# Performance work log

Measured on AMD Instinct MI355X. Metric: run time of the kernel, lower is better.

Reference implementation:

```python
import jax, jax.numpy as jnp
import numpy as np

MASS = 1.5
DT = 0.01      # physics.refresh_rate
EPS = 1e-6
B, STATE, ACT, T, H = 2048, 12, 4, 128, 512

_NORM = np.zeros(STATE, dtype=np.float32)
_NORM[0] = 4.0 / np.pi; _NORM[1] = 0.5; _NORM[2] = 4.0 / np.pi
_NORM[3] = 0.1; _NORM[4] = 1.0 / 60.0; _NORM[5] = 1.0 / 60.0
_NORM = jnp.asarray(_NORM)  # indices 6:12 stay zero (predict only normalizes 0:6)


def _leaky(x):
    return jnp.where(x >= 0, x, 0.01 * x)


def _mlp(x, W0, b0, W1, b1, W2, b2, W3, b3):
    # 3 hidden LeakyReLU layers + linear head (dropout is eval-mode identity)
    h = _leaky(x @ W0 + b0)
    h = _leaky(h @ W1 + b1)
    h = _leaky(h @ W2 + b2)
    return h @ W3 + b3


def _L_EB(phi, theta, psi):
    cph, sph = jnp.cos(phi), jnp.sin(phi)
    cth, sth = jnp.cos(theta), jnp.sin(theta)
    cps, sps = jnp.cos(psi), jnp.sin(psi)
    r1 = jnp.stack([cth * cps, sph * sth * cps - cph * sps, cph * sth * cps + sph * sps], -1)
    r2 = jnp.stack([cth * sps, sph * sth * sps + cph * cps, cph * sth * sps - sph * cps], -1)
    r3 = jnp.stack([-sth, sph * cth, cph * cth], -1)
    return jnp.stack([r1, r2, r3], -2)  # [B,3,3]


def _derivs(x, forces, I_mat, I_inv):
    V = x[:, 3:6]
    phi, theta = x[:, 6], x[:, 7]
    psi = x[:, 8]
    omega = x[:, 9:12]
    Fv, M = forces[:, 0:3], forces[:, 3:6]
    dpos = jnp.einsum('bij,bj->bi', _L_EB(phi, theta, psi), V)
    dvel = Fv / MASS - jnp.cross(omega, V)
    tth = jnp.tan(theta)
    cth = jnp.clip(jnp.cos(theta), EPS)
    sph, cph = jnp.sin(phi), jnp.cos(phi)
    one, zero = jnp.ones_like(phi), jnp.zeros_like(phi)
    J = jnp.stack([
        jnp.stack([one, sph * tth, cph * tth], -1),
        jnp.stack([zero, cph, -sph], -1),
        jnp.stack([zero, sph / cth, cph / cth], -1)], -2)  # [B,3,3]
    datt = jnp.einsum('bij,bj->bi', J, omega)
    Iw = omega @ I_mat.T                       # I @ omega
    coriolis = jnp.cross(omega, Iw)
    domega = (M - coriolis) @ I_inv.T
    return jnp.concatenate([dpos, dvel, datt, domega], axis=1)


def _rk4(x, forces, I_mat, I_inv):
    f = lambda s: _derivs(s, forces, I_mat, I_inv)
    k1 = f(x)
    k2 = f(x + 0.5 * DT * k1)
    k3 = f(x + 0.5 * DT * k2)
    k4 = f(x + DT * k3)
    return x + (DT / 6.0) * (k1 + 2 * k2 + 2 * k3 + k4)


def _predict(x, act, W, I_mat, I_inv):
    norm_x = x * _NORM
    norm_act = (act - 1500.0) / 500.0
    fn = _mlp(jnp.concatenate([norm_x, norm_act], axis=1), *W)
    zeros = jnp.zeros_like(fn[:, 0])
    forces = jnp.stack([fn[:, 0] - 0.5,
                        fn[:, 1] * -0.4 - 10.0,
                        fn[:, 2] * 0.2 - 0.1,
                        zeros, zeros, zeros], axis=1)
    return forces, _rk4(x, forces, I_mat, I_inv)


def setup_inputs() -> dict:
    key = jax.random.key(0)
    ks = jax.random.split(key, 12)
    x_t = jax.random.normal(ks[0], (B, STATE), dtype=jnp.float32) * 0.1
    act_inps = jax.random.uniform(ks[1], (B, ACT, T), dtype=jnp.float32,
                                  minval=1000.0, maxval=2000.0)
    I_mat = jnp.asarray([[0.02, 0.001, 0.002],
                         [0.001, 0.03, 0.001],
                         [0.002, 0.001, 0.04]], dtype=jnp.float32)
    def lin(k, fi, fo):
        s = np.sqrt(2.0 / (fi + fo)).astype(np.float32)
        return jax.random.normal(k, (fi, fo), dtype=jnp.float32) * s
    dims = [(STATE + ACT, H), (H, H), (H, H), (H, 6)]
    W = {}
    for i, (fi, fo) in enumerate(dims):
        W[f'W{i}'] = lin(ks[2 + i], fi, fo)
        W[f'b{i}'] = jnp.zeros((fo,), dtype=jnp.float32)
    return dict(x_t=x_t, act_inps=act_inps, I_mat=I_mat, seq_len=T, **W)


def reference(x_t, act_inps, I_mat, W0, b0, W1, b1, W2, b2, W3, b3, seq_len):
    I_inv = jnp.linalg.inv(I_mat)
    W = (W0, b0, W1, b1, W2, b2, W3, b3)
    acts = jnp.transpose(act_inps[:, :, 1:seq_len], (2, 0, 1))  # [T-1,B,ACT]

    def step(x, act):
        forces, nx = _predict(x, act, W, I_mat, I_inv)
        return nx, (forces, nx)

    _, (forces_seq, x_seq) = jax.lax.scan(step, x_t, acts)
    stacked = jnp.concatenate([x_t[:, :, None], jnp.transpose(x_seq, (1, 2, 0))], axis=2)  # [B,12,T]
    stackedForces = jnp.transpose(forces_seq, (1, 2, 0))  # [B,6,T-1]
    return stackedForces, stacked
```

## Files before the change

### kernel.cpp

```cpp
#include <hip/hip_runtime.h>
#include <stdint.h>

typedef unsigned short u16;
typedef unsigned int   u32;
typedef __attribute__((ext_vector_type(8))) short short8;
typedef __attribute__((ext_vector_type(4))) float f32x4;

#define B_TOT   2048
#define HID     512
#define T_FULL  128
#define ROWS    32
#define NWG     (B_TOT / ROWS)
#define THREADS 512
#define NT      4

#define W0F_SZ  16384
#define W1F_SZ  262144
#define W3F_SZ  8192
#define WF_TOTAL (W0F_SZ + 2*W1F_SZ + W3F_SZ)

__device__ __forceinline__ u16 f2bf(float f){
  u32 u = __float_as_uint(f);
  u32 r = (u + 0x7FFFu + ((u >> 16) & 1u)) >> 16;
  return (u16)r;
}

__device__ __forceinline__ int lds_idx(int m, int k){
  int chunk = k >> 3;
  return m * 512 + ((chunk ^ (m & 7)) << 3) + (k & 7);
}

__global__ void wm_repack(const float* __restrict__ W0, const float* __restrict__ W1,
                          const float* __restrict__ W2, const float* __restrict__ W3,
                          u16* __restrict__ wf)
{
  int idx = blockIdx.x * blockDim.x + threadIdx.x;
  if (idx >= WF_TOTAL) return;
  int e = idx;
  if (e < W0F_SZ){
    int j = e & 7, l = (e >> 3) & 63, nt = e >> 9;
    int k = ((l >> 4) << 3) + j, n = (nt << 4) + (l & 15);
    wf[idx] = (k < 16) ? f2bf(W0[k * HID + n]) : (u16)0;
    return;
  }
  e -= W0F_SZ;
  if (e < W1F_SZ){
    int j = e & 7, l = (e >> 3) & 63, rest = e >> 9, kt = rest & 15, nt = rest >> 4;
    int k = (kt << 5) + ((l >> 4) << 3) + j, n = (nt << 4) + (l & 15);
    wf[idx] = f2bf(W1[k * HID + n]);
    return;
  }
  e -= W1F_SZ;
  if (e < W1F_SZ){
    int j = e & 7, l = (e >> 3) & 63, rest = e >> 9, kt = rest & 15, nt = rest >> 4;
    int k = (kt << 5) + ((l >> 4) << 3) + j, n = (nt << 4) + (l & 15);
    wf[idx] = f2bf(W2[k * HID + n]);
    return;
  }
  e -= W1F_SZ;
  {
    int j = e & 7, l = (e >> 3) & 63, kt = e >> 9;
    int k = (kt << 5) + ((l >> 4) << 3) + j, n = l & 15;
    wf[idx] = (n < 6) ? f2bf(W3[k * 6 + n]) : (u16)0;
  }
}

__device__ __forceinline__ void invert3(const float* a, float* inv){
  float d = a[0]*(a[4]*a[8]-a[5]*a[7]) - a[1]*(a[3]*a[8]-a[5]*a[6]) + a[2]*(a[3]*a[7]-a[4]*a[6]);
  float id = 1.0f / d;
  inv[0]=(a[4]*a[8]-a[5]*a[7])*id; inv[1]=(a[2]*a[7]-a[1]*a[8])*id; inv[2]=(a[1]*a[5]-a[2]*a[4])*id;
  inv[3]=(a[5]*a[6]-a[3]*a[8])*id; inv[4]=(a[0]*a[8]-a[2]*a[6])*id; inv[5]=(a[2]*a[3]-a[0]*a[5])*id;
  inv[6]=(a[3]*a[7]-a[4]*a[6])*id; inv[7]=(a[1]*a[6]-a[0]*a[7])*id; inv[8]=(a[0]*a[4]-a[1]*a[3])*id;
}

__device__ __forceinline__ void derivs(const float* x, const float* Fv,
                                       const float* I9, const float* Ii, float* dx)
{
  float V0=x[3], V1=x[4], V2=x[5];
  float phi=x[6], th=x[7], psi=x[8];
  float w0=x[9], w1=x[10], w2=x[11];
  float sph=__sinf(phi), cph=__cosf(phi);
  float sth=__sinf(th),  cth=__cosf(th);
  float sps=__sinf(psi), cps=__cosf(psi);
  float r00=cth*cps, r01=sph*sth*cps - cph*sps, r02=cph*sth*cps + sph*sps;
  float r10=cth*sps, r11=sph*sth*sps + cph*cps, r12=cph*sth*sps - sph*cps;
  float r20=-sth,    r21=sph*cth,               r22=cph*cth;
  dx[0]=r00*V0+r01*V1+r02*V2;
  dx[1]=r10*V0+r11*V1+r12*V2;
  dx[2]=r20*V0+r21*V1+r22*V2;
  const float invm = 1.0f/1.5f;
  dx[3]=Fv[0]*invm - (w1*V2 - w2*V1);
  dx[4]=Fv[1]*invm - (w2*V0 - w0*V2);
  dx[5]=Fv[2]*invm - (w0*V1 - w1*V0);
  float tth = sth / cth;
  float rc  = 1.0f / fmaxf(cth, 1e-6f);
  dx[6]= w0 + sph*tth*w1 + cph*tth*w2;
  dx[7]=      cph*w1     - sph*w2;
  dx[8]=      sph*rc*w1  + cph*rc*w2;
  float Iw0=I9[0]*w0+I9[1]*w1+I9[2]*w2;
  float Iw1=I9[3]*w0+I9[4]*w1+I9[5]*w2;
  float Iw2=I9[6]*w0+I9[7]*w1+I9[8]*w2;
  float c0=w1*Iw2-w2*Iw1, c1=w2*Iw0-w0*Iw2, c2=w0*Iw1-w1*Iw0;
  dx[9] = -(Ii[0]*c0+Ii[1]*c1+Ii[2]*c2);
  dx[10]= -(Ii[3]*c0+Ii[4]*c1+Ii[5]*c2);
  dx[11]= -(Ii[6]*c0+Ii[7]*c1+Ii[8]*c2);
}

__device__ __forceinline__ void rk4(float* X, const float* Fv, const float* I9, const float* Ii){
  float k1[12],k2[12],k3[12],k4[12],xt[12];
  derivs(X,Fv,I9,Ii,k1);
  #pragma unroll
  for (int c=0;c<12;++c) xt[c]=X[c]+0.005f*k1[c];
  derivs(xt,Fv,I9,Ii,k2);
  #pragma unroll
  for (int c=0;c<12;++c) xt[c]=X[c]+0.005f*k2[c];
  derivs(xt,Fv,I9,Ii,k3);
  #pragma unroll
  for (int c=0;c<12;++c) xt[c]=X[c]+0.01f*k3[c];
  derivs(xt,Fv,I9,Ii,k4);
  #pragma unroll
  for (int c=0;c<12;++c) X[c]+=(0.01f/6.0f)*(k1[c]+2.0f*k2[c]+2.0f*k3[c]+k4[c]);
}

__device__ __forceinline__ void build_input(u16* bufA, const float* X,
                                            const float* __restrict__ act,
                                            int b, int r, int t)
{
  float vin[16];
  vin[0]=X[0]*1.2732395447351628f;
  vin[1]=X[1]*0.5f;
  vin[2]=X[2]*1.2732395447351628f;
  vin[3]=X[3]*0.1f;
  vin[4]=X[4]*0.016666666666666666f;
  vin[5]=X[5]*0.016666666666666666f;
  #pragma unroll
  for (int c=6;c<12;++c) vin[c]=0.0f;
  #pragma unroll
  for (int a=0;a<4;++a)
    vin[12+a] = (act[(size_t)(b*4+a)*T_FULL + t] - 1500.0f) * 0.002f;
  #pragma unroll
  for (int p=0;p<16;++p){
    u32 pack = 0u;
    if (p < 8) pack = (u32)f2bf(vin[2*p]) | ((u32)f2bf(vin[2*p+1]) << 16);
    ((u32*)bufA)[lds_idx(r, 2*p) >> 1] = pack;
  }
}

template<int KT>
__device__ __forceinline__ void do_layer(const u16* __restrict__ bufIn,
                                         const u16* __restrict__ wfrag,
                                         const float* __restrict__ bias,
                                         u16* __restrict__ bufOut,
                                         int lane, int ntb)
{
  const int lm = lane & 15, half = lane >> 4;
  const int m0 = lm, m1 = 16 + lm;
  const int sw0 = m0 & 7, sw1 = m1 & 7;
  f32x4 acc0[NT], acc1[NT];
  #pragma unroll
  for (int i=0;i<NT;++i){ acc0[i]=(f32x4)0.0f; acc1[i]=(f32x4)0.0f; }

  const u16* wbase = wfrag + (((size_t)ntb*KT*64 + lane) << 3);

  if constexpr (KT == 1){
    short8 A0 = *(const short8*)(bufIn + m0*512 + ((half ^ sw0) << 3));
    short8 A1 = *(const short8*)(bufIn + m1*512 + ((half ^ sw1) << 3));
    short8 Bf[NT];
    #pragma unroll
    for (int i=0;i<NT;++i)
      Bf[i] = *(const short8*)(wbase + ((size_t)i << 9));
    #pragma unroll
    for (int i=0;i<NT;++i){
      acc0[i] = __builtin_amdgcn_mfma_f32_16x16x32_bf16(A0, Bf[i], acc0[i], 0, 0, 0);
      acc1[i] = __builtin_amdgcn_mfma_f32_16x16x32_bf16(A1, Bf[i], acc1[i], 0, 0, 0);
    }
  } else {
    static_assert(KT == 16, "KT must be 1 or 16");
    short8 Bf[2][4][NT];
    #pragma unroll
    for (int j=0;j<4;++j)
      #pragma unroll
      for (int i=0;i<NT;++i)
        Bf[0][j][i] = *(const short8*)(wbase + ((size_t)(i*KT + j) << 9));
    #pragma unroll
    for (int blk=0; blk<4; ++blk){
      const int cur = blk & 1, nxt = cur ^ 1;
      if (blk < 3){
        #pragma unroll
        for (int j=0;j<4;++j)
          #pragma unroll
          for (int i=0;i<NT;++i)
            Bf[nxt][j][i] = *(const short8*)(wbase + ((size_t)(i*KT + blk*4 + 4 + j) << 9));
      }
      short8 A0[4], A1[4];
      #pragma unroll
      for (int j=0;j<4;++j){
        const int cb = ((blk*4 + j) << 2) + half;
        A0[j] = *(const short8*)(bufIn + m0*512 + ((cb ^ sw0) << 3));
        A1[j] = *(const short8*)(bufIn + m1*512 + ((cb ^ sw1) << 3));
      }
      #pragma unroll
      for (int j=0;j<4;++j)
        #pragma unroll
        for (int i=0;i<NT;++i){
          acc0[i] = __builtin_amdgcn_mfma_f32_16x16x32_bf16(A0[j], Bf[cur][j][i], acc0[i], 0, 0, 0);
          acc1[i] = __builtin_amdgcn_mfma_f32_16x16x32_bf16(A1[j], Bf[cur][j][i], acc1[i], 0, 0, 0);
        }
    }
  }
  #pragma unroll
  for (int i=0;i<NT;++i){
    int n = ((ntb + i) << 4) + lm;
    float bv = bias[n];
    #pragma unroll
    for (int reg=0; reg<4; ++reg){
      int r0 = (half << 2) + reg, r1 = 16 + r0;
      float v0 = acc0[i][reg] + bv; v0 = (v0 >= 0.0f) ? v0 : 0.01f*v0;
      float v1 = acc1[i][reg] + bv; v1 = (v1 >= 0.0f) ? v1 : 0.01f*v1;
      bufOut[lds_idx(r0, n)] = f2bf(v0);
      bufOut[lds_idx(r1, n)] = f2bf(v1);
    }
  }
}

__global__ __launch_bounds__(THREADS, 2)
void wm_main(const float* __restrict__ x_t, const float* __restrict__ act,
             const float* __restrict__ Imat, const int* __restrict__ seqlen_p,
             const float* __restrict__ b0, const float* __restrict__ b1,
             const float* __restrict__ b2, const float* __restrict__ b3,
             const u16* __restrict__ wf, float* __restrict__ out)
{
  __shared__ u16 bufA[16384];
  __shared__ u16 bufB[16384];
  __shared__ float xstage[32*12*32];
  __shared__ float fstage[32*6*32];
  float* fscr = (float*)(bufA + 256);

  const int tid  = threadIdx.x;
  const int lane = tid & 63;
  const int wave = tid >> 6;
  const int ntb  = wave * NT;
  const int rowbase = blockIdx.x * ROWS;
  const int steps = seqlen_p[0] - 1;
  const int seqlen = steps + 1;

  const u16* w0f = wf;
  const u16* w1f = wf + W0F_SZ;
  const u16* w2f = w1f + W1F_SZ;
  const u16* w3f = w2f + W1F_SZ;

  float* outF = out;
  float* outX = out + (size_t)B_TOT * 6 * steps;

  float X[12];
  if (tid < ROWS){
    const int b = rowbase + tid;
    #pragma unroll
    for (int c=0;c<12;++c){
      float raw = x_t[b*12 + c];
      X[c] = raw;
      outX[(size_t)(b*12 + c)*seqlen] = raw;
    }
    build_input(bufA, X, act, b, tid, 1);
  }

  for (int s=0; s<steps; ++s){
    __syncthreads();
    do_layer<1 >(bufA, w0f, b0, bufB, lane, ntb);
    __syncthreads();
    do_layer<16>(bufB, w1f, b1, bufA, lane, ntb);
    __syncthreads();
    do_layer<16>(bufA, w2f, b2, bufB, lane, ntb);
    __syncthreads();
    const int slot = s & 31;
    if (wave == 0){
      const int lm = lane & 15, half = lane >> 4;
      const int m0 = lm, m1 = 16 + lm;
      const int sw0 = m0 & 7, sw1 = m1 & 7;
      short8 w3r[16];
      #pragma unroll
      for (int kt=0; kt<16; ++kt)
        w3r[kt] = *(const short8*)(w3f + (((size_t)kt*64 + lane) << 3));
      f32x4 a3_0 = (f32x4)0.0f, a3_1 = (f32x4)0.0f;
      #pragma unroll
      for (int kt=0; kt<16; ++kt){
        int cb = (kt << 2) + half;
        short8 x0 = *(const short8*)(bufB + m0*512 + ((cb ^ sw0) << 3));
        short8 x1 = *(const short8*)(bufB + m1*512 + ((cb ^ sw1) << 3));
        a3_0 = __builtin_amdgcn_mfma_f32_16x16x32_bf16(x0, w3r[kt], a3_0, 0, 0, 0);
        a3_1 = __builtin_amdgcn_mfma_f32_16x16x32_bf16(x1, w3r[kt], a3_1, 0, 0, 0);
      }
      const int c = lm;
      float bv = (c < 6) ? b3[c] : 0.0f;
      #pragma unroll
      for (int mt=0; mt<2; ++mt){
        #pragma unroll
        for (int reg=0; reg<4; ++reg){
          int rr = (mt << 4) + (half << 2) + reg;
          float fn = ((mt == 0) ? a3_0[reg] : a3_1[reg]) + bv;
          float f;
          if      (c == 0) f = fn - 0.5f;
          else if (c == 1) f = fn * -0.4f - 10.0f;
          else if (c == 2) f = fn * 0.2f - 0.1f;
          else             f = 0.0f;
          if (c < 6) fstage[(rr*6 + c)*32 + slot] = f;
          if (c < 3) fscr[rr*3 + c] = f;
        }
      }
      asm volatile("s_waitcnt lgkmcnt(0)" ::: "memory");
      if (tid < ROWS){
        const int b = rowbase + tid;
        float I9[9], Ii[9];
        #pragma unroll
        for (int i=0;i<9;++i) I9[i] = Imat[i];
        invert3(I9, Ii);
        float Fv[3] = { fscr[tid*3], fscr[tid*3+1], fscr[tid*3+2] };
        rk4(X, Fv, I9, Ii);
        #pragma unroll
        for (int cc=0;cc<12;++cc)
          xstage[(tid*12 + cc)*32 + slot] = X[cc];
        if (s + 1 < steps) build_input(bufA, X, act, b, tid, s + 2);
      }
    }
    if (slot == 31 || s == steps - 1){
      __syncthreads();
      const int cnt = slot + 1;
      const int sBase = s - slot;
      const int so = tid & 31;
      if (so < cnt){
        for (int i = tid; i < 384*32; i += THREADS){
          int pair = i >> 5;
          int row = pair / 12, c = pair - row*12;
          outX[(size_t)((rowbase + row)*12 + c)*seqlen + sBase + 1 + so]
              = xstage[pair*32 + so];
        }
        for (int i = tid; i < 192*32; i += THREADS){
          int pair = i >> 5;
          int row = pair / 6, c = pair - row*6;
          outF[(size_t)((rowbase + row)*6 + c)*steps + sBase + so]
              = fstage[pair*32 + so];
        }
      }
    }
  }
}

extern "C" void kernel_launch(void* const* d_in, const int* in_sizes, int n_in,
                              void* d_out, int out_size, void* d_ws, size_t ws_size,
                              hipStream_t stream)
{
  const float* x_t  = (const float*)d_in[0];
  const float* act  = (const float*)d_in[1];
  const float* Imat = (const float*)d_in[2];
  const int*   seqp = (const int*)d_in[3];
  const float* W0   = (const float*)d_in[4];
  const float* b0   = (const float*)d_in[5];
  const float* W1   = (const float*)d_in[6];
  const float* b1   = (const float*)d_in[7];
  const float* W2   = (const float*)d_in[8];
  const float* b2   = (const float*)d_in[9];
  const float* W3   = (const float*)d_in[10];
  const float* b3   = (const float*)d_in[11];
  u16* wfrag = (u16*)d_ws;

  hipLaunchKernelGGL(wm_repack, dim3((WF_TOTAL + 255)/256), dim3(256), 0, stream,
                     W0, W1, W2, W3, wfrag);
  hipLaunchKernelGGL(wm_main, dim3(NWG), dim3(THREADS), 0, stream,
                     x_t, act, Imat, seqp, b0, b1, b2, b3, wfrag, (float*)d_out);
}
```

Before: 5.351 ms.

## Double threads per block, halve per-wave N tiles, use 3-deep weight prefetch

Raises the workgroup from 512 to 1024 threads so each wave owns 2 instead of 4 output column tiles. The 4-block weight double buffer becomes a per-k-step triple-buffered prefetch of B fragments, which cuts register pressure. Launch bounds are raised so more waves can be resident to hide global weight load latency. The trade is shallower prefetch per wave and more waves contending for LDS. The rest of the kernel's thread-index mapping (ROWS=32 rows, staging loops) must stay valid for 16 waves, and that code is not visible.

```diff
diff --git a/kernel.cpp b/kernel.cpp
--- a/kernel.cpp
+++ b/kernel.cpp
@@ -11,8 +11,8 @@
 #define T_FULL  128
 #define ROWS    32
 #define NWG     (B_TOT / ROWS)
-#define THREADS 512
-#define NT      4
+#define THREADS 1024
+#define NT      2
 
 #define W0F_SZ  16384
 #define W1F_SZ  262144
@@ -176,36 +176,29 @@
     }
   } else {
     static_assert(KT == 16, "KT must be 1 or 16");
-    short8 Bf[2][4][NT];
-    #pragma unroll
-    for (int j=0;j<4;++j)
+    short8 Bf[3][NT];
+    #pragma unroll
+    for (int i=0;i<NT;++i){
+      Bf[0][i] = *(const short8*)(wbase + ((size_t)(i*KT + 0) << 9));
+      Bf[1][i] = *(const short8*)(wbase + ((size_t)(i*KT + 1) << 9));
+    }
+    #pragma unroll
+    for (int kt=0; kt<KT; ++kt){
+      const int cur = kt % 3;
+      if (kt + 2 < KT){
+        const int pre = (kt + 2) % 3;
+        #pragma unroll
+        for (int i=0;i<NT;++i)
+          Bf[pre][i] = *(const short8*)(wbase + ((size_t)(i*KT + kt + 2) << 9));
+      }
+      const int cb = (kt << 2) + half;
+      short8 A0 = *(const short8*)(bufIn + m0*512 + ((cb ^ sw0) << 3));
+      short8 A1 = *(const short8*)(bufIn + m1*512 + ((cb ^ sw1) << 3));
       #pragma unroll
-      for (int i=0;i<NT;++i)
-        Bf[0][j][i] = *(const short8*)(wbase + ((size_t)(i*KT + j) << 9));
-    #pragma unroll
-    for (int blk=0; blk<4; ++blk){
-      const int cur = blk & 1, nxt = cur ^ 1;
-      if (blk < 3){
-        #pragma unroll
-        for (int j=0;j<4;++j)
-          #pragma unroll
-          for (int i=0;i<NT;++i)
-            Bf[nxt][j][i] = *(const short8*)(wbase + ((size_t)(i*KT + blk*4 + 4 + j) << 9));
-      }
-      short8 A0[4], A1[4];
-      #pragma unroll
-      for (int j=0;j<4;++j){
-        const int cb = ((blk*4 + j) << 2) + half;
-        A0[j] = *(const short8*)(bufIn + m0*512 + ((cb ^ sw0) << 3));
-        A1[j] = *(const short8*)(bufIn + m1*512 + ((cb ^ sw1) << 3));
-      }
-      #pragma unroll
-      for (int j=0;j<4;++j)
-        #pragma unroll
-        for (int i=0;i<NT;++i){
-          acc0[i] = __builtin_amdgcn_mfma_f32_16x16x32_bf16(A0[j], Bf[cur][j][i], acc0[i], 0, 0, 0);
-          acc1[i] = __builtin_amdgcn_mfma_f32_16x16x32_bf16(A1[j], Bf[cur][j][i], acc1[i], 0, 0, 0);
-        }
+      for (int i=0;i<NT;++i){
+        acc0[i] = __builtin_amdgcn_mfma_f32_16x16x32_bf16(A0, Bf[cur][i], acc0[i], 0, 0, 0);
+        acc1[i] = __builtin_amdgcn_mfma_f32_16x16x32_bf16(A1, Bf[cur][i], acc1[i], 0, 0, 0);
+      }
     }
   }
   #pragma unroll
@@ -223,7 +216,7 @@
   }
 }
 
-__global__ __launch_bounds__(THREADS, 2)
+__global__ __launch_bounds__(THREADS, 4)
 void wm_main(const float* __restrict__ x_t, const float* __restrict__ act,
              const float* __restrict__ Imat, const int* __restrict__ seqlen_p,
              const float* __restrict__ b0, const float* __restrict__ b1,
```

Result: slower. 5.674 ms (+6.0%).
